# Kernel tuning notes

Measured on AMD Instinct MI355X. Metric: run time of the kernel, lower is better.

Reference implementation:

```python
import jax, jax.numpy as jnp
import numpy as np

DIM = 256
HEADS = 8
WS = 7          # window_size
WN = 8          # window_num per side
H = W = WS * WN # 56
B = 32
MLP_HIDDEN = 4 * DIM
SCALE = (DIM // HEADS) ** -0.5
LN_EPS = 1e-5


def _rel_index(ws):
    # pairwise relative position index inside a ws x ws window (dense 0..(2ws-1)^2-1,
    # so remap_position_index is the identity relabeling)
    ch, cw = np.meshgrid(np.arange(ws), np.arange(ws), indexing='ij')
    cf = np.stack([ch.ravel(), cw.ravel()])            # (2, ws*ws)
    rel = cf[:, :, None] - cf[:, None, :]              # (2, N, N)
    rel = rel.transpose(1, 2, 0).astype(np.int32)
    rel[..., 0] += ws - 1
    rel[..., 1] += ws - 1
    rel[..., 0] *= 2 * ws - 1
    return rel.sum(-1)                                 # (N, N) in [0, (2ws-1)^2)


def _layernorm(x, g, b):
    m = x.mean(-1, keepdims=True)
    v = ((x - m) ** 2).mean(-1, keepdims=True)
    return (x - m) * jax.lax.rsqrt(v + LN_EPS) * g + b


def _mhsa(x, qkv_w, qkv_b, proj_w, proj_b, bias):
    # x: (B_, N, C); bias: (nH, N, N) or None
    B_, N, C = x.shape
    hd = C // HEADS
    qkv = (x @ qkv_w.T + qkv_b).reshape(B_, N, 3, HEADS, hd).transpose(2, 0, 3, 1, 4)
    q, k, v = qkv[0], qkv[1], qkv[2]
    attn = jnp.einsum('bhqd,bhkd->bhqk', q * SCALE, k)
    if bias is not None:
        attn = attn + bias[None]
    attn = jax.nn.softmax(attn, axis=-1)
    out = jnp.einsum('bhqk,bhkd->bhqd', attn, v).transpose(0, 2, 1, 3).reshape(B_, N, C)
    return out @ proj_w.T + proj_b


def setup_inputs() -> dict:
    key = jax.random.key(0)
    ks = jax.random.split(key, 8)
    f32 = jnp.float32
    return {
        'regional_tokens': jax.random.normal(ks[0], (B, WN * WN, DIM), f32),
        'x': jax.random.normal(ks[1], (B, H * W, DIM), f32),
        'norm1_g': jnp.ones((DIM,), f32), 'norm1_b': jnp.zeros((DIM,), f32),
        'norm2_g': jnp.ones((DIM,), f32), 'norm2_b': jnp.zeros((DIM,), f32),
        'norm3_g': jnp.ones((DIM,), f32), 'norm3_b': jnp.zeros((DIM,), f32),
        'qkv_w': jax.random.normal(ks[2], (3 * DIM, DIM), f32) * 0.02,
        'qkv_b': jnp.zeros((3 * DIM,), f32),
        'proj_w': jax.random.normal(ks[3], (DIM, DIM), f32) * 0.02,
        'proj_b': jnp.zeros((DIM,), f32),
        'bias_table': jax.random.normal(ks[4], ((2 * WS - 1) ** 2, HEADS), f32) * 0.02,
        'fc1_w': jax.random.normal(ks[5], (MLP_HIDDEN, DIM), f32) * 0.02,
        'fc1_b': jnp.zeros((MLP_HIDDEN,), f32),
        'fc2_w': jax.random.normal(ks[6], (DIM, MLP_HIDDEN), f32) * 0.02,
        'fc2_b': jnp.zeros((DIM,), f32),
        'rel_index': jnp.asarray(_rel_index(WS)),
    }


def reference(regional_tokens, x, norm1_g, norm1_b, norm2_g, norm2_b, norm3_g, norm3_b,
              qkv_w, qkv_b, proj_w, proj_b, bias_table, fc1_w, fc1_b, fc2_w, fc2_b,
              rel_index):
    Bb, L, C = x.shape
    nW = regional_tokens.shape[1]
    ws2 = WS * WS
    # --- RSA: attention over regional tokens (no relative bias) ---
    regional_tokens = regional_tokens + _mhsa(
        _layernorm(regional_tokens, norm1_g, norm1_b), qkv_w, qkv_b, proj_w, proj_b, None)
    # --- window partition of x: (B,H,W,C) -> (nW*B, ws*ws, C) (batch-major) ---
    xw = x.reshape(Bb, H // WS, WS, W // WS, WS, C)
    xw = xw.transpose(0, 1, 3, 2, 4, 5).reshape(-1, ws2, C)
    # regional tokens reshaped window-major, exactly as the torch code does
    reg = regional_tokens.transpose(1, 0, 2).reshape(nW * Bb, 1, C)
    t = jnp.concatenate([reg, xw], axis=1)  # (nW*B, 1+ws2, C)
    # --- LSA relative position bias, zero-padded for the regional token ---
    bias = bias_table[rel_index]                       # (ws2, ws2, nH)
    bias = jnp.pad(bias, ((1, 0), (1, 0), (0, 0)))      # (1+ws2, 1+ws2, nH)
    bias = bias.transpose(2, 0, 1)                      # (nH, N, N)
    t = t + _mhsa(_layernorm(t, norm2_g, norm2_b), qkv_w, qkv_b, proj_w, proj_b, bias)
    # --- MLP ---
    h = _layernorm(t, norm3_g, norm3_b)
    h = jax.nn.gelu(h @ fc1_w.T + fc1_b, approximate=False) @ fc2_w.T + fc2_b
    t = t + h
    # --- split back ---
    reg_out = t[:, 0, :].reshape(nW, Bb, C).transpose(1, 0, 2)   # (B, nW, C)
    xw = t[:, 1:, :].reshape(Bb, H // WS, W // WS, WS, WS, C)
    x_out = xw.transpose(0, 1, 3, 2, 4, 5).reshape(Bb, L, C)
    return reg_out, x_out
```

## Files before the change

### kernel.cpp

```cpp
#include <hip/hip_runtime.h>
#include <math.h>

#define SCALE_Q 0.17677669529663687f

typedef __attribute__((ext_vector_type(8))) short bf16x8;
typedef __attribute__((ext_vector_type(4))) float f32x4;
typedef __attribute__((ext_vector_type(4))) unsigned short u16x4;

static __device__ __forceinline__ unsigned short f2bf(float f) {
    unsigned int u = __float_as_uint(f);
    u += 0x7FFF + ((u >> 16) & 1);
    return (unsigned short)(u >> 16);
}

static __device__ __forceinline__ float gelu_fast(float v) {
    float s = v * (0.7978845608f + 0.0356774081f * v * v);
    float e = __expf(-2.0f * s);
    return v * __builtin_amdgcn_rcpf(1.0f + e);
}

__global__ void prep_kernel(const float* __restrict__ qkv_w, const float* __restrict__ proj_w,
                            const float* __restrict__ fc1_w, const float* __restrict__ fc2_w,
                            const float* __restrict__ bias_table, const int* __restrict__ rel_index,
                            unsigned short* __restrict__ wq, unsigned short* __restrict__ wp,
                            unsigned short* __restrict__ w1, unsigned short* __restrict__ w2,
                            float* __restrict__ bias_pad) {
    int tid = blockIdx.x * blockDim.x + threadIdx.x;
    int stride = gridDim.x * blockDim.x;
    for (int i = tid; i < 768 * 256; i += stride) wq[i] = f2bf(qkv_w[i]);
    for (int i = tid; i < 256 * 256; i += stride) wp[i] = f2bf(proj_w[i]);
    for (int i = tid; i < 1024 * 256; i += stride) w1[i] = f2bf(fc1_w[i]);
    for (int i = tid; i < 256 * 1024; i += stride) w2[i] = f2bf(fc2_w[i]);
    for (int i = tid; i < 8 * 64 * 64; i += stride) {
        int h = i >> 12, q = (i >> 6) & 63, k = i & 63;
        float v;
        if (k >= 50) v = -1e30f;
        else if (q == 0 || k == 0 || q >= 50) v = 0.f;
        else v = bias_table[rel_index[(q - 1) * 49 + (k - 1)] * 8 + h];
        bias_pad[i] = v;
    }
}

template <int IS_RSA>
__global__ __launch_bounds__(1024, 4) void attn_kernel(
    const float* __restrict__ reg_tok, const float* __restrict__ x,
    const float* __restrict__ reg2_in, float* __restrict__ out,
    const float* __restrict__ ln_g, const float* __restrict__ ln_b,
    const unsigned short* __restrict__ wq, const float* __restrict__ qkv_b,
    const unsigned short* __restrict__ wp, const float* __restrict__ proj_b,
    const float* __restrict__ bias_pad) {
    __shared__ __align__(16) unsigned char smem[140288];
    unsigned short* regA = (unsigned short*)smem;
    unsigned short* regB = (unsigned short*)(smem + 36864);
    unsigned short* vT   = (unsigned short*)(smem + 103424);

    const int tid = threadIdx.x;
    const int lane = tid & 63;
    const int wid = tid >> 6;
    const int l15 = lane & 15;
    const int lg = lane >> 4;
    const int u = blockIdx.x;
    const int NV = IS_RSA ? 64 : 50;
    const f32x4 fzero = {0.f, 0.f, 0.f, 0.f};

    int reg_off = 0, xb = 0, wi = 0, wj = 0;
    if (!IS_RSA) {
        reg_off = ((u & 31) * 64 + (u >> 5)) * 256;
        xb = u >> 6;
        int xn = u & 63;
        wi = xn >> 3; wj = xn & 7;
    }

    for (int r = wid; r < 64; r += 16) {
        if (r < NV) {
            const float* src;
            if (IS_RSA) src = reg_tok + (u * 64 + r) * 256;
            else if (r == 0) src = reg2_in + reg_off;
            else {
                int p = r - 1;
                src = x + (xb * 3136 + (wi * 7 + p / 7) * 56 + (wj * 7 + p % 7)) * 256;
            }
            f32x4 v = *(const f32x4*)(src + lane * 4);
            float s = v[0] + v[1] + v[2] + v[3];
            float s2 = v[0] * v[0] + v[1] * v[1] + v[2] * v[2] + v[3] * v[3];
            #pragma unroll
            for (int m = 1; m < 64; m <<= 1) { s += __shfl_xor(s, m); s2 += __shfl_xor(s2, m); }
            float mean = s * 0.00390625f;
            float rstd = rsqrtf(s2 * 0.00390625f - mean * mean + 1e-5f);
            u16x4 o;
            #pragma unroll
            for (int j = 0; j < 4; ++j) {
                int c = lane * 4 + j;
                o[j] = f2bf((v[j] - mean) * rstd * ln_g[c] + ln_b[c]);
            }
            *(u16x4*)(regA + r * 264 + lane * 4) = o;
        } else {
            u16x4 z = {0, 0, 0, 0};
            *(u16x4*)(regA + r * 264 + lane * 4) = z;
        }
    }
    __syncthreads();

    const int h = wid >> 1;
    const int qb = (wid & 1) * 32;

    {
        f32x4 acc[4][3];
        #pragma unroll
        for (int mi = 0; mi < 4; ++mi)
            #pragma unroll
            for (int t = 0; t < 3; ++t) acc[mi][t] = fzero;
        #pragma unroll
        for (int ks = 0; ks < 8; ++ks) {
            int k = ks * 32 + lg * 8;
            bf16x8 a[4], b[3];
            #pragma unroll
            for (int mi = 0; mi < 4; ++mi) a[mi] = *(const bf16x8*)(regA + (mi * 16 + l15) * 264 + k);
            #pragma unroll
            for (int t = 0; t < 3; ++t) b[t] = *(const bf16x8*)(wq + (wid * 48 + t * 16 + l15) * 256 + k);
            #pragma unroll
            for (int mi = 0; mi < 4; ++mi)
                #pragma unroll
                for (int t = 0; t < 3; ++t)
                    acc[mi][t] = __builtin_amdgcn_mfma_f32_16x16x32_bf16(a[mi], b[t], acc[mi][t], 0, 0, 0);
        }
        #pragma unroll
        for (int mi = 0; mi < 4; ++mi)
            #pragma unroll
            for (int t = 0; t < 3; ++t) {
                int col = wid * 48 + t * 16 + l15;
                float bias = qkv_b[col];
                #pragma unroll
                for (int r = 0; r < 4; ++r) {
                    int row = mi * 16 + lg * 4 + r;
                    unsigned short hv = f2bf(acc[mi][t][r] + bias);
                    if (col < 512) regB[row * 520 + col] = hv;
                    else vT[(col - 512) * 72 + row] = hv;
                }
            }
    }

    f32x4 bv[4][2];
    if (!IS_RSA) {
        #pragma unroll
        for (int mi = 0; mi < 4; ++mi)
            #pragma unroll
            for (int nj = 0; nj < 2; ++nj)
                bv[mi][nj] = *(const f32x4*)(bias_pad + h * 4096 + (qb + nj * 16 + l15) * 64 + mi * 16 + lg * 4);
    }
    __syncthreads();

    f32x4 st[4][2];
    {
        int k0 = h * 32 + lg * 8;
        bf16x8 af[4], bfq[2];
        #pragma unroll
        for (int mi = 0; mi < 4; ++mi) af[mi] = *(const bf16x8*)(regB + (mi * 16 + l15) * 520 + 256 + k0);
        #pragma unroll
        for (int nj = 0; nj < 2; ++nj) bfq[nj] = *(const bf16x8*)(regB + (qb + nj * 16 + l15) * 520 + k0);
        #pragma unroll
        for (int mi = 0; mi < 4; ++mi)
            #pragma unroll
            for (int nj = 0; nj < 2; ++nj)
                st[mi][nj] = __builtin_amdgcn_mfma_f32_16x16x32_bf16(af[mi], bfq[nj], fzero, 0, 0, 0);
    }

    u16x4 pf[4][2];
    #pragma unroll
    for (int nj = 0; nj < 2; ++nj) {
        float ps[4][4];
        float mx = -3.0e38f;
        #pragma unroll
        for (int mi = 0; mi < 4; ++mi)
            #pragma unroll
            for (int r = 0; r < 4; ++r) {
                float t = st[mi][nj][r] * SCALE_Q;
                if (!IS_RSA) t += bv[mi][nj][r];
                ps[mi][r] = t;
                mx = fmaxf(mx, t);
            }
        mx = fmaxf(mx, __shfl_xor(mx, 16));
        mx = fmaxf(mx, __shfl_xor(mx, 32));
        float sum = 0.f;
        #pragma unroll
        for (int mi = 0; mi < 4; ++mi)
            #pragma unroll
            for (int r = 0; r < 4; ++r) { ps[mi][r] = __expf(ps[mi][r] - mx); sum += ps[mi][r]; }
        sum += __shfl_xor(sum, 16);
        sum += __shfl_xor(sum, 32);
        float inv = __builtin_amdgcn_rcpf(sum);
        #pragma unroll
        for (int mi = 0; mi < 4; ++mi) {
            u16x4 p4;
            #pragma unroll
            for (int r = 0; r < 4; ++r) p4[r] = f2bf(ps[mi][r] * inv);
            pf[mi][nj] = p4;
        }
    }

    f32x4 ov[2][2];
    #pragma unroll
    for (int m2 = 0; m2 < 2; ++m2) { ov[m2][0] = fzero; ov[m2][1] = fzero; }
    #pragma unroll
    for (int kt = 0; kt < 4; ++kt) {
        bf16x8 pb[2];
        #pragma unroll
        for (int nj = 0; nj < 2; ++nj) {
            bf16x8 t;
            t[0] = (short)pf[kt][nj][0]; t[1] = (short)pf[kt][nj][1];
            t[2] = (short)pf[kt][nj][2]; t[3] = (short)pf[kt][nj][3];
            t[4] = 0; t[5] = 0; t[6] = 0; t[7] = 0;
            pb[nj] = t;
        }
        #pragma unroll
        for (int m2 = 0; m2 < 2; ++m2) {
            u16x4 av = *(const u16x4*)(vT + (h * 32 + m2 * 16 + l15) * 72 + kt * 16 + lg * 4);
            bf16x8 a8;
            a8[0] = (short)av[0]; a8[1] = (short)av[1]; a8[2] = (short)av[2]; a8[3] = (short)av[3];
            a8[4] = 0; a8[5] = 0; a8[6] = 0; a8[7] = 0;
            #pragma unroll
            for (int nj = 0; nj < 2; ++nj)
                ov[m2][nj] = __builtin_amdgcn_mfma_f32_16x16x32_bf16(a8, pb[nj], ov[m2][nj], 0, 0, 0);
        }
    }
    #pragma unroll
    for (int m2 = 0; m2 < 2; ++m2)
        #pragma unroll
        for (int nj = 0; nj < 2; ++nj) {
            u16x4 o4;
            #pragma unroll
            for (int r = 0; r < 4; ++r) o4[r] = f2bf(ov[m2][nj][r]);
            *(u16x4*)(regA + (qb + nj * 16 + l15) * 264 + h * 32 + m2 * 16 + lg * 4) = o4;
        }
    __syncthreads();

    {
        int nb = wid * 16;
        f32x4 acc[4];
        #pragma unroll
        for (int mi = 0; mi < 4; ++mi) acc[mi] = fzero;
        #pragma unroll
        for (int ks = 0; ks < 8; ++ks) {
            int k = ks * 32 + lg * 8;
            bf16x8 a[4], b;
            #pragma unroll
            for (int mi = 0; mi < 4; ++mi) a[mi] = *(const bf16x8*)(regA + (mi * 16 + l15) * 264 + k);
            b = *(const bf16x8*)(wp + (nb + l15) * 256 + k);
            #pragma unroll
            for (int mi = 0; mi < 4; ++mi)
                acc[mi] = __builtin_amdgcn_mfma_f32_16x16x32_bf16(a[mi], b, acc[mi], 0, 0, 0);
        }
        int col = nb + l15;
        float pb = proj_b[col];
        #pragma unroll
        for (int mi = 0; mi < 4; ++mi)
            #pragma unroll
            for (int r = 0; r < 4; ++r) {
                int row = mi * 16 + lg * 4 + r;
                if (row < NV) {
                    float val = acc[mi][r] + pb;
                    if (IS_RSA) {
                        int off = (u * 64 + row) * 256 + col;
                        out[off] = val + reg_tok[off];
                    } else if (row == 0) {
                        out[reg_off + col] = val + reg2_in[reg_off + col];
                    } else {
                        int p = row - 1;
                        int off = (xb * 3136 + (wi * 7 + p / 7) * 56 + (wj * 7 + p % 7)) * 256 + col;
                        out[524288 + off] = val + x[off];
                    }
                }
            }
    }
}

__global__ __launch_bounds__(256, 3) void mlp_kernel(
    float* __restrict__ dout,
    const float* __restrict__ ln_g, const float* __restrict__ ln_b,
    const unsigned short* __restrict__ w1, const float* __restrict__ b1,
    const unsigned short* __restrict__ w2, const float* __restrict__ b2) {
    __shared__ __align__(16) unsigned short xln[64 * 264];
    __shared__ __align__(16) unsigned short hld[64 * 136];
    const int tid = threadIdx.x;
    const int lane = tid & 63;
    const int wid = tid >> 6;
    const int l15 = lane & 15;
    const int lg = lane >> 4;
    const int row0 = blockIdx.x * 64;
    const f32x4 fzero = {0.f, 0.f, 0.f, 0.f};

    #pragma unroll
    for (int i = 0; i < 16; ++i) {
        int r = wid * 16 + i;
        f32x4 v = *(const f32x4*)(dout + (row0 + r) * 256 + lane * 4);
        float s = v[0] + v[1] + v[2] + v[3];
        float s2 = v[0] * v[0] + v[1] * v[1] + v[2] * v[2] + v[3] * v[3];
        #pragma unroll
        for (int m = 1; m < 64; m <<= 1) { s += __shfl_xor(s, m); s2 += __shfl_xor(s2, m); }
        float mean = s * 0.00390625f;
        float rstd = rsqrtf(s2 * 0.00390625f - mean * mean + 1e-5f);
        u16x4 o;
        #pragma unroll
        for (int j = 0; j < 4; ++j) {
            int c = lane * 4 + j;
            o[j] = f2bf((v[j] - mean) * rstd * ln_g[c] + ln_b[c]);
        }
        *(u16x4*)(xln + r * 264 + lane * 4) = o;
    }
    __syncthreads();

    f32x4 acc2[4][4];
    #pragma unroll
    for (int mi = 0; mi < 4; ++mi)
        #pragma unroll
        for (int ni = 0; ni < 4; ++ni) acc2[mi][ni] = fzero;

    for (int c = 0; c < 8; ++c) {
        f32x4 acc1[4][2];
        #pragma unroll
        for (int mi = 0; mi < 4; ++mi) { acc1[mi][0] = fzero; acc1[mi][1] = fzero; }
        #pragma unroll
        for (int ks = 0; ks < 8; ++ks) {
            int k = ks * 32 + lg * 8;
            bf16x8 a[4], b[2];
            #pragma unroll
            for (int mi = 0; mi < 4; ++mi)
                a[mi] = *(const bf16x8*)(xln + (mi * 16 + l15) * 264 + k);
            #pragma unroll
            for (int ni = 0; ni < 2; ++ni)
                b[ni] = *(const bf16x8*)(w1 + (c * 128 + wid * 32 + ni * 16 + l15) * 256 + k);
            #pragma unroll
            for (int mi = 0; mi < 4; ++mi)
                #pragma unroll
                for (int ni = 0; ni < 2; ++ni)
                    acc1[mi][ni] = __builtin_amdgcn_mfma_f32_16x16x32_bf16(a[mi], b[ni], acc1[mi][ni], 0, 0, 0);
        }
        #pragma unroll
        for (int mi = 0; mi < 4; ++mi)
            #pragma unroll
            for (int ni = 0; ni < 2; ++ni) {
                int hc = wid * 32 + ni * 16 + l15;
                float bb = b1[c * 128 + hc];
                #pragma unroll
                for (int r = 0; r < 4; ++r) {
                    int row = mi * 16 + lg * 4 + r;
                    float v = acc1[mi][ni][r] + bb;
                    hld[row * 136 + hc] = f2bf(gelu_fast(v));
                }
            }
        __syncthreads();
        #pragma unroll
        for (int ks = 0; ks < 4; ++ks) {
            int k = ks * 32 + lg * 8;
            bf16x8 a[4], b[4];
            #pragma unroll
            for (int mi = 0; mi < 4; ++mi)
                a[mi] = *(const bf16x8*)(hld + (mi * 16 + l15) * 136 + k);
            #pragma unroll
            for (int ni = 0; ni < 4; ++ni)
                b[ni] = *(const bf16x8*)(w2 + (wid * 64 + ni * 16 + l15) * 1024 + c * 128 + k);
            #pragma unroll
            for (int mi = 0; mi < 4; ++mi)
                #pragma unroll
                for (int ni = 0; ni < 4; ++ni)
                    acc2[mi][ni] = __builtin_amdgcn_mfma_f32_16x16x32_bf16(a[mi], b[ni], acc2[mi][ni], 0, 0, 0);
        }
        __syncthreads();
    }
    #pragma unroll
    for (int mi = 0; mi < 4; ++mi)
        #pragma unroll
        for (int ni = 0; ni < 4; ++ni) {
            int col = wid * 64 + ni * 16 + l15;
            float bb = b2[col];
            #pragma unroll
            for (int r = 0; r < 4; ++r) {
                int row = row0 + mi * 16 + lg * 4 + r;
                float* dst = dout + row * 256 + col;
                *dst = acc2[mi][ni][r] + bb + *dst;
            }
        }
}

extern "C" void kernel_launch(void* const* d_in, const int* in_sizes, int n_in,
                              void* d_out, int out_size, void* d_ws, size_t ws_size,
                              hipStream_t stream) {
    const float* regional = (const float*)d_in[0];
    const float* x = (const float*)d_in[1];
    const float* n1g = (const float*)d_in[2];
    const float* n1b = (const float*)d_in[3];
    const float* n2g = (const float*)d_in[4];
    const float* n2b = (const float*)d_in[5];
    const float* n3g = (const float*)d_in[6];
    const float* n3b = (const float*)d_in[7];
    const float* qkvw = (const float*)d_in[8];
    const float* qkvb = (const float*)d_in[9];
    const float* projw = (const float*)d_in[10];
    const float* projb = (const float*)d_in[11];
    const float* btab = (const float*)d_in[12];
    const float* f1w = (const float*)d_in[13];
    const float* f1b = (const float*)d_in[14];
    const float* f2w = (const float*)d_in[15];
    const float* f2b = (const float*)d_in[16];
    const int* relidx = (const int*)d_in[17];

    unsigned char* ws = (unsigned char*)d_ws;
    unsigned short* wq = (unsigned short*)(ws);
    unsigned short* wp = (unsigned short*)(ws + 393216);
    unsigned short* w1 = (unsigned short*)(ws + 524288);
    unsigned short* w2 = (unsigned short*)(ws + 1048576);
    float* bias_pad    = (float*)(ws + 1572864);
    float* reg2        = (float*)(ws + 1703936);

    float* out = (float*)d_out;

    prep_kernel<<<512, 256, 0, stream>>>(qkvw, projw, f1w, f2w, btab, relidx, wq, wp, w1, w2, bias_pad);
    attn_kernel<1><<<32, 1024, 0, stream>>>(regional, x, nullptr, reg2, n1g, n1b, wq, qkvb, wp, projb, nullptr);
    attn_kernel<0><<<2048, 1024, 0, stream>>>(regional, x, reg2, out, n2g, n2b, wq, qkvb, wp, projb, bias_pad);
    mlp_kernel<<<1600, 256, 0, stream>>>(out, n3g, n3b, w1, f1b, w2, f2b);
}
```

Baseline: 497.8 us.

## Prefetch weight fragments into registers ahead of MFMA loops

Weight B-fragments for the QKV, projection, and MLP GEMMs are now loaded into register arrays before they are needed: QKV weights before the LayerNorm stage, projection weights before the softmax, and the fc1/fc2 chunks for iteration c+1 during iteration c. This hides global-load latency behind other work instead of stalling each MFMA k-step on a global read. In exchange it holds many more VGPRs live (up to 32 bf16x8 fragments in the MLP), which can lower occupancy or cause spills.

Measured after the change: 891.4 us. 1.79x slower.

```diff
diff --git a/kernel.cpp b/kernel.cpp
--- a/kernel.cpp
+++ b/kernel.cpp
@@ -71,6 +71,13 @@
         wi = xn >> 3; wj = xn & 7;
     }
 
+    bf16x8 wqf[24];
+    #pragma unroll
+    for (int ks = 0; ks < 8; ++ks)
+        #pragma unroll
+        for (int t = 0; t < 3; ++t)
+            wqf[ks * 3 + t] = *(const bf16x8*)(wq + (wid * 48 + t * 16 + l15) * 256 + ks * 32 + lg * 8);
+
     for (int r = wid; r < 64; r += 16) {
         if (r < NV) {
             const float* src;
@@ -113,16 +120,14 @@
         #pragma unroll
         for (int ks = 0; ks < 8; ++ks) {
             int k = ks * 32 + lg * 8;
-            bf16x8 a[4], b[3];
+            bf16x8 a[4];
             #pragma unroll
             for (int mi = 0; mi < 4; ++mi) a[mi] = *(const bf16x8*)(regA + (mi * 16 + l15) * 264 + k);
             #pragma unroll
-            for (int t = 0; t < 3; ++t) b[t] = *(const bf16x8*)(wq + (wid * 48 + t * 16 + l15) * 256 + k);
-            #pragma unroll
             for (int mi = 0; mi < 4; ++mi)
                 #pragma unroll
                 for (int t = 0; t < 3; ++t)
-                    acc[mi][t] = __builtin_amdgcn_mfma_f32_16x16x32_bf16(a[mi], b[t], acc[mi][t], 0, 0, 0);
+                    acc[mi][t] = __builtin_amdgcn_mfma_f32_16x16x32_bf16(a[mi], wqf[ks * 3 + t], acc[mi][t], 0, 0, 0);
         }
         #pragma unroll
         for (int mi = 0; mi < 4; ++mi)
@@ -165,6 +170,11 @@
                 st[mi][nj] = __builtin_amdgcn_mfma_f32_16x16x32_bf16(af[mi], bfq[nj], fzero, 0, 0, 0);
     }
 
+    bf16x8 wpf[8];
+    #pragma unroll
+    for (int ks = 0; ks < 8; ++ks)
+        wpf[ks] = *(const bf16x8*)(wp + (wid * 16 + l15) * 256 + ks * 32 + lg * 8);
+
     u16x4 pf[4][2];
     #pragma unroll
     for (int nj = 0; nj < 2; ++nj) {
@@ -235,22 +245,20 @@
     __syncthreads();
 
     {
-        int nb = wid * 16;
         f32x4 acc[4];
         #pragma unroll
         for (int mi = 0; mi < 4; ++mi) acc[mi] = fzero;
         #pragma unroll
         for (int ks = 0; ks < 8; ++ks) {
             int k = ks * 32 + lg * 8;
-            bf16x8 a[4], b;
+            bf16x8 a[4];
             #pragma unroll
             for (int mi = 0; mi < 4; ++mi) a[mi] = *(const bf16x8*)(regA + (mi * 16 + l15) * 264 + k);
-            b = *(const bf16x8*)(wp + (nb + l15) * 256 + k);
-            #pragma unroll
-            for (int mi = 0; mi < 4; ++mi)
-                acc[mi] = __builtin_amdgcn_mfma_f32_16x16x32_bf16(a[mi], b, acc[mi], 0, 0, 0);
-        }
-        int col = nb + l15;
+            #pragma unroll
+            for (int mi = 0; mi < 4; ++mi)
+                acc[mi] = __builtin_amdgcn_mfma_f32_16x16x32_bf16(a[mi], wpf[ks], acc[mi], 0, 0, 0);
+        }
+        int col = wid * 16 + l15;
         float pb = proj_b[col];
         #pragma unroll
         for (int mi = 0; mi < 4; ++mi)
@@ -307,6 +315,18 @@
         }
         *(u16x4*)(xln + r * 264 + lane * 4) = o;
     }
+
+    bf16x8 w1f[16], w2f[16];
+    #pragma unroll
+    for (int ks = 0; ks < 8; ++ks)
+        #pragma unroll
+        for (int ni = 0; ni < 2; ++ni)
+            w1f[ks * 2 + ni] = *(const bf16x8*)(w1 + (wid * 32 + ni * 16 + l15) * 256 + ks * 32 + lg * 8);
+    #pragma unroll
+    for (int ks = 0; ks < 4; ++ks)
+        #pragma unroll
+        for (int ni = 0; ni < 4; ++ni)
+            w2f[ks * 4 + ni] = *(const bf16x8*)(w2 + (wid * 64 + ni * 16 + l15) * 1024 + ks * 32 + lg * 8);
     __syncthreads();
 
     f32x4 acc2[4][4];
@@ -322,18 +342,22 @@
         #pragma unroll
         for (int ks = 0; ks < 8; ++ks) {
             int k = ks * 32 + lg * 8;
-            bf16x8 a[4], b[2];
+            bf16x8 a[4];
             #pragma unroll
             for (int mi = 0; mi < 4; ++mi)
                 a[mi] = *(const bf16x8*)(xln + (mi * 16 + l15) * 264 + k);
             #pragma unroll
-            for (int ni = 0; ni < 2; ++ni)
-                b[ni] = *(const bf16x8*)(w1 + (c * 128 + wid * 32 + ni * 16 + l15) * 256 + k);
-            #pragma unroll
             for (int mi = 0; mi < 4; ++mi)
                 #pragma unroll
                 for (int ni = 0; ni < 2; ++ni)
-                    acc1[mi][ni] = __builtin_amdgcn_mfma_f32_16x16x32_bf16(a[mi], b[ni], acc1[mi][ni], 0, 0, 0);
+                    acc1[mi][ni] = __builtin_amdgcn_mfma_f32_16x16x32_bf16(a[mi], w1f[ks * 2 + ni], acc1[mi][ni], 0, 0, 0);
+        }
+        if (c < 7) {
+            #pragma unroll
+            for (int ks = 0; ks < 8; ++ks)
+                #pragma unroll
+                for (int ni = 0; ni < 2; ++ni)
+                    w1f[ks * 2 + ni] = *(const bf16x8*)(w1 + ((c + 1) * 128 + wid * 32 + ni * 16 + l15) * 256 + ks * 32 + lg * 8);
         }
         #pragma unroll
         for (int mi = 0; mi < 4; ++mi)
@@ -352,18 +376,22 @@
         #pragma unroll
         for (int ks = 0; ks < 4; ++ks) {
             int k = ks * 32 + lg * 8;
-            bf16x8 a[4], b[4];
+            bf16x8 a[4];
             #pragma unroll
             for (int mi = 0; mi < 4; ++mi)
                 a[mi] = *(const bf16x8*)(hld + (mi * 16 + l15) * 136 + k);
             #pragma unroll
-            for (int ni = 0; ni < 4; ++ni)
-                b[ni] = *(const bf16x8*)(w2 + (wid * 64 + ni * 16 + l15) * 1024 + c * 128 + k);
-            #pragma unroll
             for (int mi = 0; mi < 4; ++mi)
                 #pragma unroll
                 for (int ni = 0; ni < 4; ++ni)
-                    acc2[mi][ni] = __builtin_amdgcn_mfma_f32_16x16x32_bf16(a[mi], b[ni], acc2[mi][ni], 0, 0, 0);
+                    acc2[mi][ni] = __builtin_amdgcn_mfma_f32_16x16x32_bf16(a[mi], w2f[ks * 4 + ni], acc2[mi][ni], 0, 0, 0);
+        }
+        if (c < 7) {
+            #pragma unroll
+            for (int ks = 0; ks < 4; ++ks)
+                #pragma unroll
+                for (int ni = 0; ni < 4; ++ni)
+                    w2f[ks * 4 + ni] = *(const bf16x8*)(w2 + (wid * 64 + ni * 16 + l15) * 1024 + (c + 1) * 128 + ks * 32 + lg * 8);
         }
         __syncthreads();
     }
```
